# Kernel optimization log

Measured on AMD Instinct MI355X. Metric: run time of the kernel, lower is better.

The kernel has to match this reference:

```python
import math
import jax, jax.numpy as jnp
import numpy as np

B, L, D, H = 2, 2048, 1024, 16
KD = D // H


def setup_inputs() -> dict:
    key = jax.random.key(0)
    k1, k2, k3 = jax.random.split(key, 3)
    x = jax.random.normal(k1, (B, L, D), dtype=jnp.float32)
    wqkv = jax.random.normal(k2, (D, 3 * D), dtype=jnp.float32) * (1.0 / math.sqrt(D))
    wend = jax.random.normal(k3, (D, D), dtype=jnp.float32) * (1.0 / math.sqrt(D))
    return {"x": x, "wqkv": wqkv, "wend": wend}


def reference(x, wqkv, wend):
    b, l, d = x.shape
    qkv = jnp.einsum('bld,de->ble', x, wqkv)  # (B, L, 3D)
    q, k, v = jnp.split(qkv, 3, axis=-1)
    # Faithful to the torch module: reshape (B, L, D) -> (B, H, L, KD) directly.
    qh = q.reshape(b, H, l, KD)
    kh = k.reshape(b, H, l, KD)
    vh = v.reshape(b, H, l, KD)
    scores = jnp.einsum('bhqk,bhsk->bhqs', qh, kh) / math.sqrt(KD)  # (B, H, L, L)
    causal_mask = jnp.triu(jnp.ones((l, l), dtype=bool), k=1)
    scores = jnp.where(causal_mask, -jnp.inf, scores)
    probs = jax.nn.softmax(scores, axis=-1)
    attended = jnp.einsum('bhqs,bhsk->bhqk', probs, vh)  # (B, H, L, KD)
    concatted = attended.transpose(0, 2, 1, 3).reshape(b, l, d)
    return jnp.einsum('bld,de->ble', concatted, wend)
```

## Files before the change

### kernel.cpp

```cpp
#include <hip/hip_runtime.h>
#include <cstddef>
#include <cstdint>

#define L_SEQ   2048
#define D_MODEL 1024
#define NH      16
#define HKD     64
#define TD3     3072
#define NBATCH  2

typedef __attribute__((ext_vector_type(8))) short bf16x8;
typedef __attribute__((ext_vector_type(4))) float f32x4;

__device__ __forceinline__ unsigned short f2bf(float f) {
  unsigned int u = __float_as_uint(f);
  u += 0x7fffu + ((u >> 16) & 1u);
  return (unsigned short)(u >> 16);
}

__device__ __forceinline__ void gll16(const void* g, void* l) {
  __builtin_amdgcn_global_load_lds(
      (const __attribute__((address_space(1))) unsigned int*)g,
      (__attribute__((address_space(3))) unsigned int*)l, 16, 0, 0);
}

__global__ __launch_bounds__(256)
void cvt_f32_bf16(const float* __restrict__ in, unsigned short* __restrict__ out) {
  const int i = blockIdx.x * 256 + threadIdx.x;
  const float4 a = ((const float4*)in)[2 * i];
  const float4 b = ((const float4*)in)[2 * i + 1];
  bf16x8 v;
  v[0] = (short)f2bf(a.x); v[1] = (short)f2bf(a.y);
  v[2] = (short)f2bf(a.z); v[3] = (short)f2bf(a.w);
  v[4] = (short)f2bf(b.x); v[5] = (short)f2bf(b.y);
  v[6] = (short)f2bf(b.z); v[7] = (short)f2bf(b.w);
  ((bf16x8*)out)[i] = v;
}

__global__ __launch_bounds__(256)
void transpose_cvt(const float* __restrict__ W, unsigned short* __restrict__ WT,
                   int K, int N) {
  __shared__ unsigned short T[64][68];
  const int t = threadIdx.x;
  const int n0 = blockIdx.x * 64, k0 = blockIdx.y * 64;
  const int cr = t >> 4, cc = (t & 15) * 4;
#pragma unroll
  for (int i = 0; i < 4; ++i) {
    const int k = cr + 16 * i;
    const float4 v = *(const float4*)(W + (size_t)(k0 + k) * N + n0 + cc);
    T[cc + 0][k] = f2bf(v.x); T[cc + 1][k] = f2bf(v.y);
    T[cc + 2][k] = f2bf(v.z); T[cc + 3][k] = f2bf(v.w);
  }
  __syncthreads();
#pragma unroll
  for (int i = 0; i < 4; ++i) {
    const int n = cr + 16 * i;
    ushort4 o;
    o.x = T[n][cc]; o.y = T[n][cc + 1]; o.z = T[n][cc + 2]; o.w = T[n][cc + 3];
    *(ushort4*)(WT + (size_t)(n0 + n) * K + k0 + cc) = o;
  }
}

template <typename OUT>
__device__ __forceinline__ OUT cvt_out(float f);
template <> __device__ __forceinline__ float cvt_out<float>(float f) { return f; }
template <> __device__ __forceinline__ unsigned short cvt_out<unsigned short>(float f) { return f2bf(f); }

template <typename OUT>
__global__ __launch_bounds__(256)
void gemm_bf16(const unsigned short* __restrict__ A,
               const unsigned short* __restrict__ Bt,
               OUT* __restrict__ C, int M, int N, int K) {
  __shared__ unsigned short As[128 * 64];
  __shared__ unsigned short Bs[128 * 64];
  const int t = threadIdx.x, w = t >> 6, lane = t & 63;
  const int lg = lane >> 4, lq = lane & 15;
  const int m0 = blockIdx.y * 128, n0 = blockIdx.x * 128;
  const int wr = w >> 1, wc = w & 1;

  f32x4 acc[4][4];
#pragma unroll
  for (int a = 0; a < 4; ++a)
#pragma unroll
    for (int b = 0; b < 4; ++b) acc[a][b] = (f32x4)0.f;

  for (int k0 = 0; k0 < K; k0 += 64) {
    __syncthreads();
#pragma unroll
    for (int i = 0; i < 4; ++i) {
      const int c = 256 * i + t;
      const int row = c >> 3, cc = (c & 7) * 8;
      gll16(A + (size_t)(m0 + row) * K + k0 + cc,
            (char*)As + (256 * i + 64 * w) * 16);
      gll16(Bt + (size_t)(n0 + row) * K + k0 + cc,
            (char*)Bs + (256 * i + 64 * w) * 16);
    }
    __syncthreads();
#pragma unroll
    for (int ks = 0; ks < 2; ++ks) {
      bf16x8 af[4], bfr[4];
#pragma unroll
      for (int mf = 0; mf < 4; ++mf)
        af[mf] = *(const bf16x8*)((const char*)As +
                   (wr * 64 + mf * 16 + lq) * 128 + ks * 64 + lg * 16);
#pragma unroll
      for (int nf = 0; nf < 4; ++nf)
        bfr[nf] = *(const bf16x8*)((const char*)Bs +
                   (wc * 64 + nf * 16 + lq) * 128 + ks * 64 + lg * 16);
#pragma unroll
      for (int mf = 0; mf < 4; ++mf)
#pragma unroll
        for (int nf = 0; nf < 4; ++nf)
          acc[mf][nf] = __builtin_amdgcn_mfma_f32_16x16x32_bf16(
              af[mf], bfr[nf], acc[mf][nf], 0, 0, 0);
    }
  }

#pragma unroll
  for (int mf = 0; mf < 4; ++mf)
#pragma unroll
    for (int nf = 0; nf < 4; ++nf) {
      const int col = n0 + wc * 64 + nf * 16 + lq;
#pragma unroll
      for (int r = 0; r < 4; ++r) {
        const int row = m0 + wr * 64 + mf * 16 + lg * 4 + r;
        C[(size_t)row * N + col] = cvt_out<OUT>(acc[mf][nf][r]);
      }
    }
}

__device__ __forceinline__ size_t head_row(int part, int b, int h, int s) {
  return ((size_t)(b * L_SEQ + h * 128 + (s >> 4))) * TD3 +
         (size_t)part * D_MODEL + (size_t)(s & 15) * HKD;
}

__global__ __launch_bounds__(256)
void transpose_v(const unsigned short* __restrict__ qkv,
                 unsigned short* __restrict__ vT) {
  __shared__ unsigned short T[64][68];
  const int t = threadIdx.x;
  const int kt = blockIdx.x, bh = blockIdx.y, b = bh >> 4, h = bh & 15;
  const int s0 = kt * 64;
  const int sr = t >> 4, c4 = (t & 15) * 4;
#pragma unroll
  for (int i = 0; i < 4; ++i) {
    const int s = sr + 16 * i;
    const ushort4 v = *(const ushort4*)(qkv + head_row(2, b, h, s0 + s) + c4);
    T[c4 + 0][s] = v.x; T[c4 + 1][s] = v.y;
    T[c4 + 2][s] = v.z; T[c4 + 3][s] = v.w;
  }
  __syncthreads();
#pragma unroll
  for (int i = 0; i < 4; ++i) {
    const int d = sr + 16 * i;
    ushort4 o;
    o.x = T[d][c4]; o.y = T[d][c4 + 1]; o.z = T[d][c4 + 2]; o.w = T[d][c4 + 3];
    *(ushort4*)(vT + ((size_t)(bh * 64 + d)) * L_SEQ + s0 + c4) = o;
  }
}

__global__ __launch_bounds__(512)
void attn_mfma(const unsigned short* __restrict__ qkv,
               const unsigned short* __restrict__ vT,
               unsigned short* __restrict__ concat) {
  __shared__ unsigned short Ks[2][64 * 64];
  __shared__ unsigned short Vs[2][64 * 64];
  __shared__ unsigned short Pl[8][16][72];

  const int t = threadIdx.x, w = t >> 6, lane = t & 63;
  const int lg = lane >> 4, lq = lane & 15;
  const int qt = 15 - blockIdx.x;
  const int bh = blockIdx.y, b = bh >> 4, h = bh & 15;
  const int q0 = qt * 128;
  const int qrow = q0 + w * 16 + lq;

  bf16x8 qf[2];
  {
    const size_t qb = head_row(0, b, h, qrow) + lg * 8;
    qf[0] = *(const bf16x8*)(qkv + qb);
    qf[1] = *(const bf16x8*)(qkv + qb + 32);
  }

  const int skey = t >> 3, sdc = t & 7;
  const int swz = (sdc ^ (skey & 7)) * 8;
  const size_t kSrc0 = head_row(1, b, h, skey) + swz;
  const size_t vSrc0 = ((size_t)(bh * 64 + skey)) * L_SEQ + swz;
  char* const kDst = (char*)&Ks[0][0] + w * 1024;
  char* const vDst = (char*)&Vs[0][0] + w * 1024;

  f32x4 o[4];
#pragma unroll
  for (int mf = 0; mf < 4; ++mf) o[mf] = (f32x4)0.f;
  float mrun = -1e30f, lrun = 0.f;

  const int ktmax = 2 * qt + 1;

  gll16(qkv + kSrc0, kDst);
  gll16(vT + vSrc0, vDst);

  for (int kt = 0; kt <= ktmax; ++kt) {
    const int k0 = kt * 64;
    const int cur = kt & 1;
    __syncthreads();

    if (kt < ktmax) {
      gll16(qkv + kSrc0 + (size_t)(k0 + 64) * 192, kDst + (1 - cur) * 8192);
      gll16(vT + vSrc0 + (size_t)(k0 + 64), vDst + (1 - cur) * 8192);
    }
    const char* kb = (const char*)&Ks[cur][0];
    const char* vb = (const char*)&Vs[cur][0];

    f32x4 s[4];
#pragma unroll
    for (int mf = 0; mf < 4; ++mf) s[mf] = (f32x4)0.f;
    __builtin_amdgcn_s_setprio(1);
#pragma unroll
    for (int ks = 0; ks < 2; ++ks) {
      bf16x8 kf[4];
#pragma unroll
      for (int mf = 0; mf < 4; ++mf) {
        const int key = mf * 16 + lq;
        const int chunk = (lg + 4 * ks) ^ (key & 7);
        kf[mf] = *(const bf16x8*)(kb + key * 128 + chunk * 16);
      }
#pragma unroll
      for (int mf = 0; mf < 4; ++mf)
        s[mf] = __builtin_amdgcn_mfma_f32_16x16x32_bf16(kf[mf], qf[ks], s[mf], 0, 0, 0);
    }
    __builtin_amdgcn_s_setprio(0);

    float sv[16];
    float tmax = -1e30f;
#pragma unroll
    for (int mf = 0; mf < 4; ++mf)
#pragma unroll
      for (int r = 0; r < 4; ++r) {
        float x = s[mf][r] * 0.125f;
        if (k0 + mf * 16 + lg * 4 + r > qrow) x = -1e30f;
        sv[mf * 4 + r] = x;
        tmax = fmaxf(tmax, x);
      }
    tmax = fmaxf(tmax, __shfl_xor(tmax, 16));
    tmax = fmaxf(tmax, __shfl_xor(tmax, 32));
    const float mnew = fmaxf(mrun, tmax);
    const float sc = __expf(mrun - mnew);
    float rs = 0.f;
#pragma unroll
    for (int mf = 0; mf < 4; ++mf) {
      const float p0 = __expf(sv[mf * 4 + 0] - mnew);
      const float p1 = __expf(sv[mf * 4 + 1] - mnew);
      const float p2 = __expf(sv[mf * 4 + 2] - mnew);
      const float p3 = __expf(sv[mf * 4 + 3] - mnew);
      rs += (p0 + p1) + (p2 + p3);
      ushort4 pk;
      pk.x = f2bf(p0); pk.y = f2bf(p1); pk.z = f2bf(p2); pk.w = f2bf(p3);
      *(ushort4*)&Pl[w][lq][mf * 16 + lg * 4] = pk;
    }
    rs += __shfl_xor(rs, 16);
    rs += __shfl_xor(rs, 32);
    lrun = lrun * sc + rs;
    mrun = mnew;
#pragma unroll
    for (int mf = 0; mf < 4; ++mf) {
      o[mf][0] *= sc; o[mf][1] *= sc; o[mf][2] *= sc; o[mf][3] *= sc;
    }

    __builtin_amdgcn_s_setprio(1);
#pragma unroll
    for (int ks = 0; ks < 2; ++ks) {
      const bf16x8 pf = *(const bf16x8*)&Pl[w][lq][ks * 32 + lg * 8];
      bf16x8 vf[4];
#pragma unroll
      for (int mf = 0; mf < 4; ++mf) {
        const int d = mf * 16 + lq;
        const int chunk = (lg + 4 * ks) ^ (d & 7);
        vf[mf] = *(const bf16x8*)(vb + d * 128 + chunk * 16);
      }
#pragma unroll
      for (int mf = 0; mf < 4; ++mf)
        o[mf] = __builtin_amdgcn_mfma_f32_16x16x32_bf16(vf[mf], pf, o[mf], 0, 0, 0);
    }
    __builtin_amdgcn_s_setprio(0);
  }

  const float inv = 1.f / lrun;
#pragma unroll
  for (int mf = 0; mf < 4; ++mf) {
    ushort4 ov;
    ov.x = f2bf(o[mf][0] * inv); ov.y = f2bf(o[mf][1] * inv);
    ov.z = f2bf(o[mf][2] * inv); ov.w = f2bf(o[mf][3] * inv);
    *(ushort4*)(concat + (size_t)(b * L_SEQ + qrow) * D_MODEL + h * HKD +
                mf * 16 + lg * 4) = ov;
  }
}

extern "C" void kernel_launch(void* const* d_in, const int* in_sizes, int n_in,
                              void* d_out, int out_size, void* d_ws, size_t ws_size,
                              hipStream_t stream) {
  const float* x    = (const float*)d_in[0];
  const float* wqkv = (const float*)d_in[1];
  const float* wend = (const float*)d_in[2];
  float* out = (float*)d_out;

  char* ws = (char*)d_ws;
  unsigned short* qkv   = (unsigned short*)(ws);
  unsigned short* xb    = (unsigned short*)(ws + 25165824);
  unsigned short* wqkvT = (unsigned short*)(ws + 33554432);
  unsigned short* wendT = (unsigned short*)(ws + 39845888);
  unsigned short* cat   = (unsigned short*)(ws + 41943040);
  unsigned short* vT    = xb;

  cvt_f32_bf16<<<2048, 256, 0, stream>>>(x, xb);
  transpose_cvt<<<dim3(48, 16), 256, 0, stream>>>(wqkv, wqkvT, 1024, 3072);
  transpose_cvt<<<dim3(16, 16), 256, 0, stream>>>(wend, wendT, 1024, 1024);

  gemm_bf16<unsigned short><<<dim3(24, 32), 256, 0, stream>>>(
      xb, wqkvT, qkv, 4096, 3072, 1024);
  transpose_v<<<dim3(32, 32), 256, 0, stream>>>(qkv, vT);
  attn_mfma<<<dim3(16, 32), 512, 0, stream>>>(qkv, vT, cat);
  gemm_bf16<float><<<dim3(8, 32), 256, 0, stream>>>(
      cat, wendT, out, 4096, 1024, 1024);
}
```

Before: 235.1 us.

## Shrink attention tiles, fold scale into Q, lazy rescale, remap GEMM blocks

```diff
diff --git a/kernel.cpp b/kernel.cpp
--- a/kernel.cpp
+++ b/kernel.cpp
@@ -1,4 +1,5 @@
 #include <hip/hip_runtime.h>
+#include <hip/hip_bf16.h>
 #include <cstddef>
 #include <cstdint>
 
@@ -16,6 +17,12 @@
   unsigned int u = __float_as_uint(f);
   u += 0x7fffu + ((u >> 16) & 1u);
   return (unsigned short)(u >> 16);
+}
+
+__device__ __forceinline__ unsigned int pk2bf(float a, float b) {
+  union { __hip_bfloat162 h; unsigned int u; } cv;
+  cv.h = __float22bfloat162_rn(make_float2(a, b));
+  return cv.u;
 }
 
 __device__ __forceinline__ void gll16(const void* g, void* l) {
@@ -75,7 +82,11 @@
   __shared__ unsigned short Bs[128 * 64];
   const int t = threadIdx.x, w = t >> 6, lane = t & 63;
   const int lg = lane >> 4, lq = lane & 15;
-  const int m0 = blockIdx.y * 128, n0 = blockIdx.x * 128;
+
+  const int nwg = gridDim.x * gridDim.y;
+  int bid = blockIdx.y * gridDim.x + blockIdx.x;
+  bid = (bid & 7) * (nwg >> 3) + (bid >> 3);
+  const int m0 = (bid / gridDim.x) * 128, n0 = (bid % gridDim.x) * 128;
   const int wr = w >> 1, wc = w & 1;
 
   f32x4 acc[4][4];
@@ -159,19 +170,21 @@
   }
 }
 
-__global__ __launch_bounds__(512)
+#define QK_SCALE 0.18033688011112043f
+
+__global__ __launch_bounds__(256)
 void attn_mfma(const unsigned short* __restrict__ qkv,
                const unsigned short* __restrict__ vT,
                unsigned short* __restrict__ concat) {
   __shared__ unsigned short Ks[2][64 * 64];
   __shared__ unsigned short Vs[2][64 * 64];
-  __shared__ unsigned short Pl[8][16][72];
+  __shared__ unsigned short Pl[4][16][72];
 
   const int t = threadIdx.x, w = t >> 6, lane = t & 63;
   const int lg = lane >> 4, lq = lane & 15;
-  const int qt = 15 - blockIdx.x;
+  const int qt = 31 - blockIdx.x;
   const int bh = blockIdx.y, b = bh >> 4, h = bh & 15;
-  const int q0 = qt * 128;
+  const int q0 = qt * 64;
   const int qrow = q0 + w * 16 + lq;
 
   bf16x8 qf[2];
@@ -179,12 +192,25 @@
     const size_t qb = head_row(0, b, h, qrow) + lg * 8;
     qf[0] = *(const bf16x8*)(qkv + qb);
     qf[1] = *(const bf16x8*)(qkv + qb + 32);
-  }
-
-  const int skey = t >> 3, sdc = t & 7;
-  const int swz = (sdc ^ (skey & 7)) * 8;
-  const size_t kSrc0 = head_row(1, b, h, skey) + swz;
-  const size_t vSrc0 = ((size_t)(bh * 64 + skey)) * L_SEQ + swz;
+#pragma unroll
+    for (int s = 0; s < 2; ++s)
+#pragma unroll
+      for (int j = 0; j < 8; ++j) {
+        const float f =
+            __uint_as_float(((unsigned int)(unsigned short)qf[s][j]) << 16);
+        qf[s][j] = (short)f2bf(f * QK_SCALE);
+      }
+  }
+
+  const int srow = t >> 3;
+  const int swz = ((t & 7) ^ (srow & 7)) * 8;
+  size_t kSrc[2], vSrc[2];
+#pragma unroll
+  for (int i = 0; i < 2; ++i) {
+    const int skey = 32 * i + srow;
+    kSrc[i] = head_row(1, b, h, skey) + swz;
+    vSrc[i] = ((size_t)(bh * 64 + skey)) * L_SEQ + swz;
+  }
   char* const kDst = (char*)&Ks[0][0] + w * 1024;
   char* const vDst = (char*)&Vs[0][0] + w * 1024;
 
@@ -193,19 +219,24 @@
   for (int mf = 0; mf < 4; ++mf) o[mf] = (f32x4)0.f;
   float mrun = -1e30f, lrun = 0.f;
 
-  const int ktmax = 2 * qt + 1;
-
-  gll16(qkv + kSrc0, kDst);
-  gll16(vT + vSrc0, vDst);
-
-  for (int kt = 0; kt <= ktmax; ++kt) {
+#pragma unroll
+  for (int i = 0; i < 2; ++i) {
+    gll16(qkv + kSrc[i], kDst + i * 4096);
+    gll16(vT + vSrc[i], vDst + i * 4096);
+  }
+
+  for (int kt = 0; kt <= qt; ++kt) {
     const int k0 = kt * 64;
     const int cur = kt & 1;
     __syncthreads();
 
-    if (kt < ktmax) {
-      gll16(qkv + kSrc0 + (size_t)(k0 + 64) * 192, kDst + (1 - cur) * 8192);
-      gll16(vT + vSrc0 + (size_t)(k0 + 64), vDst + (1 - cur) * 8192);
+    if (kt < qt) {
+      const int nb = (1 - cur) * 8192;
+#pragma unroll
+      for (int i = 0; i < 2; ++i) {
+        gll16(qkv + kSrc[i] + (size_t)(k0 + 64) * 192, kDst + nb + i * 4096);
+        gll16(vT + vSrc[i] + (size_t)(k0 + 64), vDst + nb + i * 4096);
+      }
     }
     const char* kb = (const char*)&Ks[cur][0];
     const char* vb = (const char*)&Vs[cur][0];
@@ -230,40 +261,57 @@
     __builtin_amdgcn_s_setprio(0);
 
     float sv[16];
-    float tmax = -1e30f;
-#pragma unroll
-    for (int mf = 0; mf < 4; ++mf)
-#pragma unroll
-      for (int r = 0; r < 4; ++r) {
-        float x = s[mf][r] * 0.125f;
-        if (k0 + mf * 16 + lg * 4 + r > qrow) x = -1e30f;
-        sv[mf * 4 + r] = x;
-        tmax = fmaxf(tmax, x);
-      }
+    if (kt == qt) {
+      const int th = w * 16 + lq;
+#pragma unroll
+      for (int mf = 0; mf < 4; ++mf)
+#pragma unroll
+        for (int r = 0; r < 4; ++r) {
+          float x = s[mf][r];
+          if (mf * 16 + lg * 4 + r > th) x = -1e30f;
+          sv[mf * 4 + r] = x;
+        }
+    } else {
+#pragma unroll
+      for (int mf = 0; mf < 4; ++mf)
+#pragma unroll
+        for (int r = 0; r < 4; ++r) sv[mf * 4 + r] = s[mf][r];
+    }
+    float t0 = fmaxf(fmaxf(sv[0], sv[1]), fmaxf(sv[2], sv[3]));
+    float t1 = fmaxf(fmaxf(sv[4], sv[5]), fmaxf(sv[6], sv[7]));
+    float t2 = fmaxf(fmaxf(sv[8], sv[9]), fmaxf(sv[10], sv[11]));
+    float t3 = fmaxf(fmaxf(sv[12], sv[13]), fmaxf(sv[14], sv[15]));
+    float tmax = fmaxf(fmaxf(t0, t1), fmaxf(t2, t3));
     tmax = fmaxf(tmax, __shfl_xor(tmax, 16));
     tmax = fmaxf(tmax, __shfl_xor(tmax, 32));
-    const float mnew = fmaxf(mrun, tmax);
-    const float sc = __expf(mrun - mnew);
+
+    if (!__all(tmax - mrun <= 8.f)) {
+      const float mnew = fmaxf(mrun, tmax);
+      const float sc = __builtin_amdgcn_exp2f(mrun - mnew);
+      lrun *= sc;
+#pragma unroll
+      for (int mf = 0; mf < 4; ++mf) {
+        o[mf][0] *= sc; o[mf][1] *= sc; o[mf][2] *= sc; o[mf][3] *= sc;
+      }
+      mrun = mnew;
+    }
+
     float rs = 0.f;
 #pragma unroll
     for (int mf = 0; mf < 4; ++mf) {
-      const float p0 = __expf(sv[mf * 4 + 0] - mnew);
-      const float p1 = __expf(sv[mf * 4 + 1] - mnew);
-      const float p2 = __expf(sv[mf * 4 + 2] - mnew);
-      const float p3 = __expf(sv[mf * 4 + 3] - mnew);
+      const float p0 = __builtin_amdgcn_exp2f(sv[mf * 4 + 0] - mrun);
+      const float p1 = __builtin_amdgcn_exp2f(sv[mf * 4 + 1] - mrun);
+      const float p2 = __builtin_amdgcn_exp2f(sv[mf * 4 + 2] - mrun);
+      const float p3 = __builtin_amdgcn_exp2f(sv[mf * 4 + 3] - mrun);
       rs += (p0 + p1) + (p2 + p3);
-      ushort4 pk;
-      pk.x = f2bf(p0); pk.y = f2bf(p1); pk.z = f2bf(p2); pk.w = f2bf(p3);
-      *(ushort4*)&Pl[w][lq][mf * 16 + lg * 4] = pk;
+      uint2 pk;
+      pk.x = pk2bf(p0, p1);
+      pk.y = pk2bf(p2, p3);
+      *(uint2*)&Pl[w][lq][mf * 16 + lg * 4] = pk;
     }
     rs += __shfl_xor(rs, 16);
     rs += __shfl_xor(rs, 32);
-    lrun = lrun * sc + rs;
-    mrun = mnew;
-#pragma unroll
-    for (int mf = 0; mf < 4; ++mf) {
-      o[mf][0] *= sc; o[mf][1] *= sc; o[mf][2] *= sc; o[mf][3] *= sc;
-    }
+    lrun += rs;
 
     __builtin_amdgcn_s_setprio(1);
 #pragma unroll
@@ -286,11 +334,11 @@
   const float inv = 1.f / lrun;
 #pragma unroll
   for (int mf = 0; mf < 4; ++mf) {
-    ushort4 ov;
-    ov.x = f2bf(o[mf][0] * inv); ov.y = f2bf(o[mf][1] * inv);
-    ov.z = f2bf(o[mf][2] * inv); ov.w = f2bf(o[mf][3] * inv);
-    *(ushort4*)(concat + (size_t)(b * L_SEQ + qrow) * D_MODEL + h * HKD +
-                mf * 16 + lg * 4) = ov;
+    uint2 ov;
+    ov.x = pk2bf(o[mf][0] * inv, o[mf][1] * inv);
+    ov.y = pk2bf(o[mf][2] * inv, o[mf][3] * inv);
+    *(uint2*)(concat + (size_t)(b * L_SEQ + qrow) * D_MODEL + h * HKD +
+              mf * 16 + lg * 4) = ov;
   }
 }
 
@@ -317,7 +365,7 @@
   gemm_bf16<unsigned short><<<dim3(24, 32), 256, 0, stream>>>(
       xb, wqkvT, qkv, 4096, 3072, 1024);
   transpose_v<<<dim3(32, 32), 256, 0, stream>>>(qkv, vT);
-  attn_mfma<<<dim3(16, 32), 512, 0, stream>>>(qkv, vT, cat);
+  attn_mfma<<<dim3(32, 32), 256, 0, stream>>>(qkv, vT, cat);
   gemm_bf16<float><<<dim3(8, 32), 256, 0, stream>>>(
       cat, wendT, out, 4096, 1024, 1024);
 }
```

New measurement: 248.5 us. 1.06x slower.
